# Kernel optimization log

Hardware: AMD Instinct MI355X
Metric: run time of the kernel (lower is better)

Reference implementation:

```python
import jax, jax.numpy as jnp
import numpy as np

B, S, D, H = 32, 512, 512, 8
DF = D // H  # dim_feature = 64
NEG_INF = -1e32


def setup_inputs() -> dict:
    key = jax.random.key(0)
    ks = jax.random.split(key, 8)
    std = 1.0 / np.sqrt(D)  # xavier-ish scale for square linears
    return {
        "q": jax.random.normal(ks[0], (B, S, D), jnp.float32),
        "k": jax.random.normal(ks[1], (B, S, D), jnp.float32),
        "v": jax.random.normal(ks[2], (B, S, D), jnp.float32),
        "mask": jnp.tril(jnp.ones((S, S), jnp.int32))[None, None],  # causal AKT mask
        "zero_pad": 1,
        "question_difficulty_emb": jax.random.normal(ks[3], (B, S, S), jnp.float32) * 0.1,
        "Wk": jax.random.normal(ks[4], (D, D), jnp.float32) * std,
        "bk": jnp.zeros((D,), jnp.float32),
        "Wv": jax.random.normal(ks[5], (D, D), jnp.float32) * std,
        "bv": jnp.zeros((D,), jnp.float32),
        "Wo": jax.random.normal(ks[6], (D, D), jnp.float32) * std,
        "bo": jnp.zeros((D,), jnp.float32),
        "gammas": jax.random.normal(ks[7], (H, 1, 1), jnp.float32) * 0.1,
    }


def reference(q, k, v, mask, zero_pad, question_difficulty_emb, Wk, bk, Wv, bv, Wo, bo, gammas):
    bs = q.shape[0]

    def proj(x, W, b):
        # Linear then split heads: [B,S,D] -> [B,H,S,DF]
        return (x @ W.T + b).reshape(bs, -1, H, DF).transpose(0, 2, 1, 3)

    qh = proj(q, Wk, bk)  # key_query_same=True: q uses key_linear
    kh = proj(k, Wk, bk)
    vh = proj(v, Wv, bv)

    scores = jnp.einsum("bhqd,bhkd->bhqk", qh, kh) / jnp.sqrt(jnp.float32(DF))
    seqlen = scores.shape[-1]
    maskb = mask == 0  # [1,1,S,S]

    # --- distance-decay term (computed under no_grad in torch, detached) ---
    scores_ = jax.nn.softmax(jnp.where(maskb, NEG_INF, scores), axis=-1)
    scores_ = scores_ * mask.astype(scores.dtype)
    distcum = jnp.cumsum(scores_, axis=-1)                      # [B,H,S,S]
    disttot = jnp.sum(scores_, axis=-1, keepdims=True)          # [B,H,S,1]
    pos = jnp.abs(jnp.arange(seqlen)[None, :] - jnp.arange(seqlen)[:, None]).astype(scores.dtype)
    dist_scores = jnp.sqrt(jnp.clip((disttot - distcum) * pos[None, None], 0.0))
    dist_scores = jax.lax.stop_gradient(dist_scores)

    gamma = -jax.nn.softplus(gammas)[None]                      # [1,H,1,1]
    diff = jnp.exp(jax.nn.sigmoid(question_difficulty_emb))[:, None]  # [B,1,S,S]
    total_effect = jnp.clip(jnp.exp(dist_scores * gamma * diff), 1e-5, 1e5)

    scores = scores * total_effect
    scores = jax.nn.softmax(jnp.where(maskb, NEG_INF, scores), axis=-1)
    if zero_pad:
        scores = scores.at[:, :, 0, :].set(0.0)  # zero first query row
    scores = jnp.where(maskb, 0.0, scores)
    # dropout p=0 (eval) -> identity

    out = jnp.einsum("bhqk,bhkd->bhqd", scores, vh)
    concat = out.transpose(0, 2, 1, 3).reshape(bs, -1, D)
    return concat @ Wo.T + bo
```

## Files before the change

kernel.cpp:

```cpp
#include <hip/hip_runtime.h>

typedef unsigned short u16;
typedef __attribute__((ext_vector_type(8))) short short8;
typedef __attribute__((ext_vector_type(4))) float f32x4;

__device__ __forceinline__ float b2f(u16 u) {
    return __uint_as_float(((unsigned int)u) << 16);
}
__device__ __forceinline__ u16 f2b(float f) {
    unsigned int x = __float_as_uint(f);
    return (u16)((x + 0x7FFFu + ((x >> 16) & 1u)) >> 16);
}
__device__ __forceinline__ float ldf(const void* p, size_t i, bool f32) {
    return f32 ? ((const float*)p)[i] : b2f(((const u16*)p)[i]);
}
__device__ __forceinline__ void stf(void* p, size_t i, bool f32, float v) {
    if (f32) ((float*)p)[i] = v; else ((u16*)p)[i] = f2b(v);
}

__global__ void detect_f32(const u16* __restrict__ q, int* __restrict__ flag) {
    __shared__ int cw, cz;
    if (threadIdx.x == 0) { cw = 0; cz = 0; }
    __syncthreads();
    int w = 0, z = 0;
    for (int i = threadIdx.x; i < 4096; i += 256) {
        u16 u = q[i];
        int e = (u >> 7) & 0xFF;
        if (e >= 0xC8) w++;
        if (((i & 1) == 0) && u == 0) z++;
    }
    atomicAdd(&cw, w); atomicAdd(&cz, z);
    __syncthreads();
    if (threadIdx.x == 0) *flag = (cw > 8 || cz > 1024) ? 1 : 0;
}

__global__ __launch_bounds__(256) void cvt_w3(
    const void* __restrict__ w0, const void* __restrict__ w1,
    const void* __restrict__ w2, u16* __restrict__ d0, u16* __restrict__ d1,
    u16* __restrict__ d2, int n, const int* __restrict__ flag)
{
    const bool f32 = (*flag) != 0;
    const int z = blockIdx.y;
    const void* src = (z == 0) ? w0 : (z == 1) ? w1 : w2;
    u16* dst = (z == 0) ? d0 : (z == 1) ? d1 : d2;
    const int i = (blockIdx.x * 256 + threadIdx.x) * 8;
    if (i >= n) return;
    short8 o;
    if (f32) {
        const float4* s = (const float4*)((const float*)src + i);
        float4 v0 = s[0], v1 = s[1];
        o[0] = (short)f2b(v0.x); o[1] = (short)f2b(v0.y);
        o[2] = (short)f2b(v0.z); o[3] = (short)f2b(v0.w);
        o[4] = (short)f2b(v1.x); o[5] = (short)f2b(v1.y);
        o[6] = (short)f2b(v1.z); o[7] = (short)f2b(v1.w);
    } else {
        o = *(const short8*)((const u16*)src + i);
    }
    *(short8*)(dst + i) = o;
}

#define BM 128
#define BN 128
#define BK 32
#define LSTR 40

template<int ASRC>
__device__ __forceinline__ void gemm_body(
    const void* __restrict__ A, const u16* __restrict__ W,
    const void* __restrict__ bias, void* __restrict__ dst,
    bool f32, int mode, int bm, int bn, int M, int N, int K)
{
    __shared__ u16 As[BM * LSTR];
    __shared__ u16 Bs[BN * LSTR];
    const int t = threadIdx.x;
    const int w = t >> 6, l = t & 63, lq = l & 15, quad = l >> 4;
    const int wr = (w >> 1) * 64, wc = (w & 1) * 64;
    const int srow = t >> 1;
    const int scol = (t & 1) * 16;

    f32x4 acc[4][4] = {};

    for (int k0 = 0; k0 < K; k0 += BK) {
        const size_t ai = (size_t)(bm + srow) * K + k0 + scol;
        short8 a0, a1;
        if (ASRC == 1 && f32) {
            const float4* ap = (const float4*)((const float*)A + ai);
            float4 f0 = ap[0], f1 = ap[1], f2 = ap[2], f3 = ap[3];
            a0[0] = (short)f2b(f0.x); a0[1] = (short)f2b(f0.y);
            a0[2] = (short)f2b(f0.z); a0[3] = (short)f2b(f0.w);
            a0[4] = (short)f2b(f1.x); a0[5] = (short)f2b(f1.y);
            a0[6] = (short)f2b(f1.z); a0[7] = (short)f2b(f1.w);
            a1[0] = (short)f2b(f2.x); a1[1] = (short)f2b(f2.y);
            a1[2] = (short)f2b(f2.z); a1[3] = (short)f2b(f2.w);
            a1[4] = (short)f2b(f3.x); a1[5] = (short)f2b(f3.y);
            a1[6] = (short)f2b(f3.z); a1[7] = (short)f2b(f3.w);
        } else {
            a0 = *(const short8*)((const u16*)A + ai);
            a1 = *(const short8*)((const u16*)A + ai + 8);
        }
        short8 b0 = *(const short8*)&W[(size_t)(bn + srow) * K + k0 + scol];
        short8 b1 = *(const short8*)&W[(size_t)(bn + srow) * K + k0 + scol + 8];
        __syncthreads();
        *(short8*)&As[srow * LSTR + scol]     = a0;
        *(short8*)&As[srow * LSTR + scol + 8] = a1;
        *(short8*)&Bs[srow * LSTR + scol]     = b0;
        *(short8*)&Bs[srow * LSTR + scol + 8] = b1;
        __syncthreads();
        short8 af[4], bf[4];
        #pragma unroll
        for (int i = 0; i < 4; ++i)
            af[i] = *(const short8*)&As[(wr + i * 16 + lq) * LSTR + quad * 8];
        #pragma unroll
        for (int j = 0; j < 4; ++j)
            bf[j] = *(const short8*)&Bs[(wc + j * 16 + lq) * LSTR + quad * 8];
        #pragma unroll
        for (int i = 0; i < 4; ++i)
            #pragma unroll
            for (int j = 0; j < 4; ++j)
                acc[i][j] = __builtin_amdgcn_mfma_f32_16x16x32_bf16(
                    af[i], bf[j], acc[i][j], 0, 0, 0);
    }

    #pragma unroll
    for (int j = 0; j < 4; ++j) {
        const int n = bn + wc + j * 16 + lq;
        const float bb = ldf(bias, n, f32);
        #pragma unroll
        for (int i = 0; i < 4; ++i) {
            #pragma unroll
            for (int r = 0; r < 4; ++r) {
                const int m = bm + wr + i * 16 + quad * 4 + r;
                const float vout = acc[i][j][r] + bb;
                if (mode == 0) {
                    const int b = m >> 9, s = m & 511, hh = n >> 6, df = n & 63;
                    ((u16*)dst)[((((size_t)b * 8 + hh) * 512 + s) << 6) + df] = f2b(vout);
                } else if (mode == 2) {
                    const int b = m >> 9, s = m & 511, hh = n >> 6, df = n & 63;
                    ((u16*)dst)[((((size_t)b * 8 + hh) * 64 + df) << 9) + s] = f2b(vout);
                } else {
                    stf(dst, (size_t)m * N + n, f32, vout);
                }
            }
        }
    }
}

__global__ __launch_bounds__(256) void proj3(
    const void* __restrict__ Aq, const void* __restrict__ Ak,
    const void* __restrict__ Av, const u16* __restrict__ cWk,
    const u16* __restrict__ cWv, const void* __restrict__ bk,
    const void* __restrict__ bv, u16* __restrict__ qh, u16* __restrict__ kh,
    u16* __restrict__ vt, const int* __restrict__ flag, int M, int N, int K)
{
    const bool f32 = (*flag) != 0;
    const int z = blockIdx.z;
    const void* A = (z == 0) ? Aq : (z == 1) ? Ak : Av;
    const u16* W = (z < 2) ? cWk : cWv;
    const void* bias = (z < 2) ? bk : bv;
    void* dst = (z == 0) ? (void*)qh : (z == 1) ? (void*)kh : (void*)vt;
    const int mode = (z < 2) ? 0 : 2;
    gemm_body<1>(A, W, bias, dst, f32, mode, blockIdx.y * BM, blockIdx.x * BN, M, N, K);
}

__global__ __launch_bounds__(256) void gemm_out(
    const u16* __restrict__ A, const u16* __restrict__ W,
    const void* __restrict__ bias, void* __restrict__ dst,
    const int* __restrict__ flag, int M, int N, int K)
{
    gemm_body<0>(A, W, bias, dst, (*flag) != 0, 1, blockIdx.y * BM, blockIdx.x * BN, M, N, K);
}

#define QT  16
#define SRS 577
#define PRS 584

__global__ __launch_bounds__(512) void akt_attn(
    const u16* __restrict__ qh, const u16* __restrict__ kh,
    const u16* __restrict__ vt, const void* __restrict__ qde,
    const void* __restrict__ gammas, const int* __restrict__ zero_pad,
    const int* __restrict__ flag, u16* __restrict__ attn)
{
    __shared__ _Float16 s_h[QT * SRS];
    __shared__ u16      p_lds[QT * PRS];

    const int blk = blockIdx.x;
    const int xcd = blk & 7;
    const int i0  = blk >> 3;
    const int qt  = i0 & 31;
    const int grp = i0 >> 5;
    const int h = xcd, b = grp;

    const int q0 = qt * QT;
    const int t = threadIdx.x, w = t >> 6, l = t & 63;
    const int lq = l & 15, quad = l >> 4;
    const bool f32 = (*flag) != 0;
    const size_t bh = ((size_t)b * 8 + h) * 512;
    const int qmax = q0 + QT - 1;

    {
        const u16* qb = qh + (bh + q0) * 64;
        short8 af0 = *(const short8*)(qb + lq * 64 +      quad * 8);
        short8 af1 = *(const short8*)(qb + lq * 64 + 32 + quad * 8);
        const u16* kb = kh + bh * 64;
        const int KT = (q0 + QT + 127) >> 7;
        int n0 = w * 16;
        bool act = (n0 <= qmax);
        short8 bf0, bf1;
        if (act) {
            bf0 = *(const short8*)(kb + (size_t)(n0 + lq) * 64 +      quad * 8);
            bf1 = *(const short8*)(kb + (size_t)(n0 + lq) * 64 + 32 + quad * 8);
        }
        for (int kt = 0; kt < KT; ++kt) {
            const int n0n = (kt + 1) * 128 + w * 16;
            const bool actn = (kt + 1 < KT) && (n0n <= qmax);
            short8 nb0, nb1;
            if (actn) {
                nb0 = *(const short8*)(kb + (size_t)(n0n + lq) * 64 +      quad * 8);
                nb1 = *(const short8*)(kb + (size_t)(n0n + lq) * 64 + 32 + quad * 8);
            }
            if (act) {
                f32x4 acc = {0.f, 0.f, 0.f, 0.f};
                acc = __builtin_amdgcn_mfma_f32_16x16x32_bf16(af0, bf0, acc, 0, 0, 0);
                acc = __builtin_amdgcn_mfma_f32_16x16x32_bf16(af1, bf1, acc, 0, 0, 0);
                const int col = n0 + lq;
                const int cm  = col + (col >> 3);
                #pragma unroll
                for (int r = 0; r < 4; ++r)
                    s_h[(quad * 4 + r) * SRS + cm] = (_Float16)(acc[r] * 0.125f);
            }
            bf0 = nb0; bf1 = nb1; act = actn; n0 = n0n;
        }
    }
    __syncthreads();

    {
        const float gma = -log1pf(expf(ldf(gammas, h, f32)));
        const int zp = zero_pad[0];
        const int c0 = l * 8;
        #pragma unroll
        for (int rr = 0; rr < 2; ++rr) {
            const int row = w * 2 + rr;
            const int q = q0 + row;
            const _Float16* srow = s_h + row * SRS + l * 9;
            float s[8];
            #pragma unroll
            for (int j = 0; j < 8; ++j)
                s[j] = (c0 + j <= q) ? (float)srow[j] : -1e30f;
            float cs[8]; float run = 0.f;
            #pragma unroll
            for (int j = 0; j < 8; ++j) { float p = __expf(s[j]); run += p; cs[j] = run; }
            float incl = run;
            #pragma unroll
            for (int o = 1; o < 64; o <<= 1) {
                float u = __shfl_up(incl, o, 64);
                if (l >= o) incl += u;
            }
            const float ls   = __shfl(incl, 63, 64);
            const float inv1 = __builtin_amdgcn_rcpf(ls);
            const float exclr = incl - run;
            float x[8];
            const size_t qoff = ((size_t)b * 512 + q) * 512 + c0;
            if (c0 <= q) {
                if (f32) {
                    const float* qp = (const float*)qde + qoff;
                    #pragma unroll
                    for (int j = 0; j < 8; ++j) x[j] = qp[j];
                } else {
                    short8 v8 = *(const short8*)((const u16*)qde + qoff);
                    #pragma unroll
                    for (int j = 0; j < 8; ++j) x[j] = b2f((u16)v8[j]);
                }
            } else {
                #pragma unroll
                for (int j = 0; j < 8; ++j) x[j] = 0.f;
            }
            float f8[8]; float lf = 0.f;
            #pragma unroll
            for (int j = 0; j < 8; ++j) {
                float dc   = (exclr + cs[j]) * inv1;
                float rem  = 1.f - dc;
                float pos  = (float)(q - (c0 + j));
                float dist = __builtin_amdgcn_sqrtf(fmaxf(rem * pos, 0.f));
                float sig  = __builtin_amdgcn_rcpf(1.f + __expf(-x[j]));
                float eff  = __expf(dist * gma * __expf(sig));
                eff = fminf(fmaxf(eff, 1e-5f), 1e5f);
                float s2 = (c0 + j <= q) ? s[j] * eff : -1e30f;
                float f = __expf(s2);
                f8[j] = f; lf += f;
            }
            #pragma unroll
            for (int o = 32; o > 0; o >>= 1) lf += __shfl_xor(lf, o, 64);
            float inv2 = __builtin_amdgcn_rcpf(lf);
            if (zp && q == 0) inv2 = 0.f;
            short8 pb;
            #pragma unroll
            for (int j = 0; j < 8; ++j) pb[j] = (short)f2b(f8[j] * inv2);
            *(short8*)(p_lds + row * PRS + c0 + 8 * (l >> 3)) = pb;
        }
    }
    __syncthreads();

    if (w < 4) {
        const int g = w;
        const int KS = (qmax >> 5) + 1;
        const u16* vb = vt + ((size_t)(b * 8 + h) * 64 + g * 16 + lq) * 512;
        const u16* prow = p_lds + lq * PRS;
        f32x4 oacc = {0.f, 0.f, 0.f, 0.f};
        int kb2 = quad * 8;
        short8 pa = *(const short8*)(prow + kb2 + 8 * (kb2 >> 6));
        short8 vv = *(const short8*)(vb + kb2);
        for (int ks = 0; ks < KS; ++ks) {
            short8 pan, vvn;
            const int kn = (ks + 1) * 32 + quad * 8;
            if (ks + 1 < KS) {
                pan = *(const short8*)(prow + kn + 8 * (kn >> 6));
                vvn = *(const short8*)(vb + kn);
            }
            oacc = __builtin_amdgcn_mfma_f32_16x16x32_bf16(pa, vv, oacc, 0, 0, 0);
            pa = pan; vv = vvn;
        }
        const size_t ob = ((size_t)b * 512 + q0 + quad * 4) * 512 + h * 64 + g * 16 + lq;
        #pragma unroll
        for (int r = 0; r < 4; ++r)
            attn[ob + (size_t)r * 512] = f2b(oacc[r]);
    }
}

extern "C" void kernel_launch(void* const* d_in, const int* in_sizes, int n_in,
                              void* d_out, int out_size, void* d_ws, size_t ws_size,
                              hipStream_t stream) {
    const void* q   = d_in[0];
    const void* k   = d_in[1];
    const void* v   = d_in[2];
    const int*  zp  = (const int*)d_in[4];
    const void* qde = d_in[5];
    const void* Wk  = d_in[6];
    const void* bk  = d_in[7];
    const void* Wv  = d_in[8];
    const void* bv  = d_in[9];
    const void* Wo  = d_in[10];
    const void* bo  = d_in[11];
    const void* gam = d_in[12];

    const int M = 32 * 512, N = 512, K = 512;
    const int NW = 512 * 512;

    char* ws = (char*)d_ws;
    int*  flag = (int*)ws;
    const size_t SZB = (size_t)M * K * 2;
    const size_t SZW = (size_t)NW * 2;
    u16* cWk  = (u16*)(ws + 1024);
    u16* cWv  = (u16*)(ws + 1024 + SZW);
    u16* cWo  = (u16*)(ws + 1024 + 2 * SZW);
    u16* qh   = (u16*)(ws + 1024 + 3 * SZW);
    u16* kh   = (u16*)(ws + 1024 + 3 * SZW + SZB);
    u16* vt   = (u16*)(ws + 1024 + 3 * SZW + 2 * SZB);
    u16* attn = (u16*)(ws + 1024 + 3 * SZW + 3 * SZB);

    detect_f32<<<1, 256, 0, stream>>>((const u16*)q, flag);
    cvt_w3<<<dim3(NW / 2048, 3), 256, 0, stream>>>(Wk, Wv, Wo, cWk, cWv, cWo, NW, flag);
    proj3<<<dim3(N / BN, M / BM, 3), 256, 0, stream>>>(
        q, k, v, cWk, cWv, bk, bv, qh, kh, vt, flag, M, N, K);
    akt_attn<<<8192, 512, 0, stream>>>(qh, kh, vt, qde, gam, zp, flag, attn);
    gemm_out<<<dim3(N / BN, M / BM), 256, 0, stream>>>(attn, cWo, bo, d_out, flag, M, N, K);
}
```

Measured before the change: 412.6 us.

## Pre-convert activations, use direct global-to-LDS loads, split PV across all waves

Adds a separate conversion pass that turns q/k/v into bf16 buffers. This lets the GEMM tiles load through global_load_lds straight into unpadded LDS, with no per-element conversion in registers. In the attention kernel, the difficulty-embedding load is hoisted and vectorized unconditionally, and the score LDS stride and padding scheme change. The PV matmul is split across all 8 waves, with the two partial sums reduced through shared memory. In exchange it costs an extra full read and write pass over the inputs, unpadded LDS tiles that may bank-conflict, and one more barrier.

```diff
diff --git a/kernel.cpp b/kernel.cpp
--- a/kernel.cpp
+++ b/kernel.cpp
@@ -2,6 +2,7 @@
 
 typedef unsigned short u16;
 typedef __attribute__((ext_vector_type(8))) short short8;
+typedef __attribute__((ext_vector_type(8))) _Float16 h8;
 typedef __attribute__((ext_vector_type(4))) float f32x4;
 
 __device__ __forceinline__ float b2f(u16 u) {
@@ -16,6 +17,12 @@
 }
 __device__ __forceinline__ void stf(void* p, size_t i, bool f32, float v) {
     if (f32) ((float*)p)[i] = v; else ((u16*)p)[i] = f2b(v);
+}
+
+__device__ __forceinline__ void ldsld16(const void* g, void* l) {
+    __builtin_amdgcn_global_load_lds(
+        (const __attribute__((address_space(1))) unsigned int*)g,
+        (__attribute__((address_space(3))) unsigned int*)l, 16, 0, 0);
 }
 
 __global__ void detect_f32(const u16* __restrict__ q, int* __restrict__ flag) {
@@ -34,14 +41,14 @@
     if (threadIdx.x == 0) *flag = (cw > 8 || cz > 1024) ? 1 : 0;
 }
 
-__global__ __launch_bounds__(256) void cvt_w3(
-    const void* __restrict__ w0, const void* __restrict__ w1,
-    const void* __restrict__ w2, u16* __restrict__ d0, u16* __restrict__ d1,
+__global__ __launch_bounds__(256) void cvt3(
+    const void* __restrict__ s0, const void* __restrict__ s1,
+    const void* __restrict__ s2, u16* __restrict__ d0, u16* __restrict__ d1,
     u16* __restrict__ d2, int n, const int* __restrict__ flag)
 {
     const bool f32 = (*flag) != 0;
-    const int z = blockIdx.y;
-    const void* src = (z == 0) ? w0 : (z == 1) ? w1 : w2;
+    const int z = blockIdx.z;
+    const void* src = (z == 0) ? s0 : (z == 1) ? s1 : s2;
     u16* dst = (z == 0) ? d0 : (z == 1) ? d1 : d2;
     const int i = (blockIdx.x * 256 + threadIdx.x) * 8;
     if (i >= n) return;
@@ -62,57 +69,42 @@
 #define BM 128
 #define BN 128
 #define BK 32
-#define LSTR 40
-
-template<int ASRC>
+
 __device__ __forceinline__ void gemm_body(
-    const void* __restrict__ A, const u16* __restrict__ W,
+    const u16* __restrict__ A, const u16* __restrict__ W,
     const void* __restrict__ bias, void* __restrict__ dst,
     bool f32, int mode, int bm, int bn, int M, int N, int K)
 {
-    __shared__ u16 As[BM * LSTR];
-    __shared__ u16 Bs[BN * LSTR];
+    __shared__ u16 As[BM * BK];
+    __shared__ u16 Bs[BN * BK];
     const int t = threadIdx.x;
     const int w = t >> 6, l = t & 63, lq = l & 15, quad = l >> 4;
     const int wr = (w >> 1) * 64, wc = (w & 1) * 64;
-    const int srow = t >> 1;
-    const int scol = (t & 1) * 16;
+
+    const int whalf = (w & 1) * 64;
+    const u16* gsrc = (w < 2) ? A : W;
+    const int  gbase = (w < 2) ? bm : bn;
+    u16* lbase = (w < 2) ? As : Bs;
 
     f32x4 acc[4][4] = {};
 
     for (int k0 = 0; k0 < K; k0 += BK) {
-        const size_t ai = (size_t)(bm + srow) * K + k0 + scol;
-        short8 a0, a1;
-        if (ASRC == 1 && f32) {
-            const float4* ap = (const float4*)((const float*)A + ai);
-            float4 f0 = ap[0], f1 = ap[1], f2 = ap[2], f3 = ap[3];
-            a0[0] = (short)f2b(f0.x); a0[1] = (short)f2b(f0.y);
-            a0[2] = (short)f2b(f0.z); a0[3] = (short)f2b(f0.w);
-            a0[4] = (short)f2b(f1.x); a0[5] = (short)f2b(f1.y);
-            a0[6] = (short)f2b(f1.z); a0[7] = (short)f2b(f1.w);
-            a1[0] = (short)f2b(f2.x); a1[1] = (short)f2b(f2.y);
-            a1[2] = (short)f2b(f2.z); a1[3] = (short)f2b(f2.w);
-            a1[4] = (short)f2b(f3.x); a1[5] = (short)f2b(f3.y);
-            a1[6] = (short)f2b(f3.z); a1[7] = (short)f2b(f3.w);
-        } else {
-            a0 = *(const short8*)((const u16*)A + ai);
-            a1 = *(const short8*)((const u16*)A + ai + 8);
-        }
-        short8 b0 = *(const short8*)&W[(size_t)(bn + srow) * K + k0 + scol];
-        short8 b1 = *(const short8*)&W[(size_t)(bn + srow) * K + k0 + scol + 8];
         __syncthreads();
-        *(short8*)&As[srow * LSTR + scol]     = a0;
-        *(short8*)&As[srow * LSTR + scol + 8] = a1;
-        *(short8*)&Bs[srow * LSTR + scol]     = b0;
-        *(short8*)&Bs[srow * LSTR + scol + 8] = b1;
+        #pragma unroll
+        for (int c = 0; c < 4; ++c) {
+            const int row = whalf + c * 16 + (l >> 2);
+            ldsld16(gsrc + (size_t)(gbase + row) * K + k0 + (l & 3) * 8,
+                    lbase + row * BK + (l & 3) * 8);
+        }
+        asm volatile("s_waitcnt vmcnt(0)" ::: "memory");
         __syncthreads();
         short8 af[4], bf[4];
         #pragma unroll
         for (int i = 0; i < 4; ++i)
-            af[i] = *(const short8*)&As[(wr + i * 16 + lq) * LSTR + quad * 8];
+            af[i] = *(const short8*)&As[(wr + i * 16 + lq) * BK + quad * 8];
         #pragma unroll
         for (int j = 0; j < 4; ++j)
-            bf[j] = *(const short8*)&Bs[(wc + j * 16 + lq) * LSTR + quad * 8];
+            bf[j] = *(const short8*)&Bs[(wc + j * 16 + lq) * BK + quad * 8];
         #pragma unroll
         for (int i = 0; i < 4; ++i)
             #pragma unroll
@@ -146,20 +138,19 @@
 }
 
 __global__ __launch_bounds__(256) void proj3(
-    const void* __restrict__ Aq, const void* __restrict__ Ak,
-    const void* __restrict__ Av, const u16* __restrict__ cWk,
+    const u16* __restrict__ cq, const u16* __restrict__ ck,
+    const u16* __restrict__ cv, const u16* __restrict__ cWk,
     const u16* __restrict__ cWv, const void* __restrict__ bk,
     const void* __restrict__ bv, u16* __restrict__ qh, u16* __restrict__ kh,
     u16* __restrict__ vt, const int* __restrict__ flag, int M, int N, int K)
 {
-    const bool f32 = (*flag) != 0;
     const int z = blockIdx.z;
-    const void* A = (z == 0) ? Aq : (z == 1) ? Ak : Av;
+    const u16* A = (z == 0) ? cq : (z == 1) ? ck : cv;
     const u16* W = (z < 2) ? cWk : cWv;
     const void* bias = (z < 2) ? bk : bv;
     void* dst = (z == 0) ? (void*)qh : (z == 1) ? (void*)kh : (void*)vt;
-    const int mode = (z < 2) ? 0 : 2;
-    gemm_body<1>(A, W, bias, dst, f32, mode, blockIdx.y * BM, blockIdx.x * BN, M, N, K);
+    gemm_body(A, W, bias, dst, (*flag) != 0, (z < 2) ? 0 : 2,
+              blockIdx.y * BM, blockIdx.x * BN, M, N, K);
 }
 
 __global__ __launch_bounds__(256) void gemm_out(
@@ -167,11 +158,12 @@
     const void* __restrict__ bias, void* __restrict__ dst,
     const int* __restrict__ flag, int M, int N, int K)
 {
-    gemm_body<0>(A, W, bias, dst, (*flag) != 0, 1, blockIdx.y * BM, blockIdx.x * BN, M, N, K);
+    gemm_body(A, W, bias, dst, (*flag) != 0, 1,
+              blockIdx.y * BM, blockIdx.x * BN, M, N, K);
 }
 
 #define QT  16
-#define SRS 577
+#define SRS 568
 #define PRS 584
 
 __global__ __launch_bounds__(512) void akt_attn(
@@ -184,11 +176,10 @@
     __shared__ u16      p_lds[QT * PRS];
 
     const int blk = blockIdx.x;
-    const int xcd = blk & 7;
-    const int i0  = blk >> 3;
-    const int qt  = i0 & 31;
-    const int grp = i0 >> 5;
-    const int h = xcd, b = grp;
+    const int h = blk & 7;
+    const int i0 = blk >> 3;
+    const int qt = i0 & 31;
+    const int b = i0 >> 5;
 
     const int q0 = qt * QT;
     const int t = threadIdx.x, w = t >> 6, l = t & 63;
@@ -222,8 +213,7 @@
                 f32x4 acc = {0.f, 0.f, 0.f, 0.f};
                 acc = __builtin_amdgcn_mfma_f32_16x16x32_bf16(af0, bf0, acc, 0, 0, 0);
                 acc = __builtin_amdgcn_mfma_f32_16x16x32_bf16(af1, bf1, acc, 0, 0, 0);
-                const int col = n0 + lq;
-                const int cm  = col + (col >> 3);
+                const int cm = n0 + lq + 8 * (n0 >> 6);
                 #pragma unroll
                 for (int r = 0; r < 4; ++r)
                     s_h[(quad * 4 + r) * SRS + cm] = (_Float16)(acc[r] * 0.125f);
@@ -241,11 +231,23 @@
         for (int rr = 0; rr < 2; ++rr) {
             const int row = w * 2 + rr;
             const int q = q0 + row;
-            const _Float16* srow = s_h + row * SRS + l * 9;
+            float x[8];
+            const size_t qoff = ((size_t)b * 512 + q) * 512 + c0;
+            if (f32) {
+                const float4* qp = (const float4*)((const float*)qde + qoff);
+                float4 x0 = qp[0], x1 = qp[1];
+                x[0] = x0.x; x[1] = x0.y; x[2] = x0.z; x[3] = x0.w;
+                x[4] = x1.x; x[5] = x1.y; x[6] = x1.z; x[7] = x1.w;
+            } else {
+                short8 v8 = *(const short8*)((const u16*)qde + qoff);
+                #pragma unroll
+                for (int j = 0; j < 8; ++j) x[j] = b2f((u16)v8[j]);
+            }
+            h8 sv = *(const h8*)(s_h + row * SRS + l * 8 + 8 * (l >> 3));
             float s[8];
             #pragma unroll
             for (int j = 0; j < 8; ++j)
-                s[j] = (c0 + j <= q) ? (float)srow[j] : -1e30f;
+                s[j] = (c0 + j <= q) ? (float)sv[j] : -1e30f;
             float cs[8]; float run = 0.f;
             #pragma unroll
             for (int j = 0; j < 8; ++j) { float p = __expf(s[j]); run += p; cs[j] = run; }
@@ -258,22 +260,6 @@
             const float ls   = __shfl(incl, 63, 64);
             const float inv1 = __builtin_amdgcn_rcpf(ls);
             const float exclr = incl - run;
-            float x[8];
-            const size_t qoff = ((size_t)b * 512 + q) * 512 + c0;
-            if (c0 <= q) {
-                if (f32) {
-                    const float* qp = (const float*)qde + qoff;
-                    #pragma unroll
-                    for (int j = 0; j < 8; ++j) x[j] = qp[j];
-                } else {
-                    short8 v8 = *(const short8*)((const u16*)qde + qoff);
-                    #pragma unroll
-                    for (int j = 0; j < 8; ++j) x[j] = b2f((u16)v8[j]);
-                }
-            } else {
-                #pragma unroll
-                for (int j = 0; j < 8; ++j) x[j] = 0.f;
-            }
             float f8[8]; float lf = 0.f;
             #pragma unroll
             for (int j = 0; j < 8; ++j) {
@@ -300,29 +286,33 @@
     }
     __syncthreads();
 
-    if (w < 4) {
-        const int g = w;
+    {
+        const int g = w & 3;
+        const int half = w >> 2;
         const int KS = (qmax >> 5) + 1;
         const u16* vb = vt + ((size_t)(b * 8 + h) * 64 + g * 16 + lq) * 512;
         const u16* prow = p_lds + lq * PRS;
         f32x4 oacc = {0.f, 0.f, 0.f, 0.f};
-        int kb2 = quad * 8;
-        short8 pa = *(const short8*)(prow + kb2 + 8 * (kb2 >> 6));
-        short8 vv = *(const short8*)(vb + kb2);
-        for (int ks = 0; ks < KS; ++ks) {
-            short8 pan, vvn;
-            const int kn = (ks + 1) * 32 + quad * 8;
-            if (ks + 1 < KS) {
-                pan = *(const short8*)(prow + kn + 8 * (kn >> 6));
-                vvn = *(const short8*)(vb + kn);
-            }
+        for (int ks = half; ks < KS; ks += 2) {
+            const int kb2 = ks * 32 + quad * 8;
+            short8 pa = *(const short8*)(prow + kb2 + 8 * (kb2 >> 6));
+            short8 vv = *(const short8*)(vb + kb2);
             oacc = __builtin_amdgcn_mfma_f32_16x16x32_bf16(pa, vv, oacc, 0, 0, 0);
-            pa = pan; vv = vvn;
-        }
-        const size_t ob = ((size_t)b * 512 + q0 + quad * 4) * 512 + h * 64 + g * 16 + lq;
-        #pragma unroll
-        for (int r = 0; r < 4; ++r)
-            attn[ob + (size_t)r * 512] = f2b(oacc[r]);
+        }
+        float* opart = (float*)s_h;
+        if (half == 1) {
+            #pragma unroll
+            for (int r = 0; r < 4; ++r)
+                opart[(g * 16 + quad * 4 + r) * 17 + lq] = oacc[r];
+        }
+        __syncthreads();
+        if (half == 0) {
+            const size_t ob = ((size_t)b * 512 + q0 + quad * 4) * 512 + h * 64 + g * 16 + lq;
+            #pragma unroll
+            for (int r = 0; r < 4; ++r)
+                attn[ob + (size_t)r * 512] =
+                    f2b(oacc[r] + opart[(g * 16 + quad * 4 + r) * 17 + lq]);
+        }
     }
 }
 
@@ -343,24 +333,29 @@
     const void* gam = d_in[12];
 
     const int M = 32 * 512, N = 512, K = 512;
+    const int NBIG = M * K;
     const int NW = 512 * 512;
 
     char* ws = (char*)d_ws;
-    int*  flag = (int*)ws;
-    const size_t SZB = (size_t)M * K * 2;
+    int* flag = (int*)ws;
+    const size_t SZB = (size_t)NBIG * 2;
     const size_t SZW = (size_t)NW * 2;
     u16* cWk  = (u16*)(ws + 1024);
     u16* cWv  = (u16*)(ws + 1024 + SZW);
     u16* cWo  = (u16*)(ws + 1024 + 2 * SZW);
-    u16* qh   = (u16*)(ws + 1024 + 3 * SZW);
-    u16* kh   = (u16*)(ws + 1024 + 3 * SZW + SZB);
-    u16* vt   = (u16*)(ws + 1024 + 3 * SZW + 2 * SZB);
-    u16* attn = (u16*)(ws + 1024 + 3 * SZW + 3 * SZB);
+    u16* cq   = (u16*)(ws + 1024 + 3 * SZW);
+    u16* ck   = (u16*)(ws + 1024 + 3 * SZW + SZB);
+    u16* cv   = (u16*)(ws + 1024 + 3 * SZW + 2 * SZB);
+    u16* qh   = (u16*)(ws + 1024 + 3 * SZW + 3 * SZB);
+    u16* kh   = (u16*)(ws + 1024 + 3 * SZW + 4 * SZB);
+    u16* vt   = (u16*)(ws + 1024 + 3 * SZW + 5 * SZB);
+    u16* attn = (u16*)(ws + 1024 + 3 * SZW + 6 * SZB);
 
     detect_f32<<<1, 256, 0, stream>>>((const u16*)q, flag);
-    cvt_w3<<<dim3(NW / 2048, 3), 256, 0, stream>>>(Wk, Wv, Wo, cWk, cWv, cWo, NW, flag);
+    cvt3<<<dim3(NW / 2048, 1, 3), 256, 0, stream>>>(Wk, Wv, Wo, cWk, cWv, cWo, NW, flag);
+    cvt3<<<dim3(NBIG / 2048, 1, 3), 256, 0, stream>>>(q, k, v, cq, ck, cv, NBIG, flag);
     proj3<<<dim3(N / BN, M / BM, 3), 256, 0, stream>>>(
-        q, k, v, cWk, cWv, bk, bv, qh, kh, vt, flag, M, N, K);
+        cq, ck, cv, cWk, cWv, bk, bv, qh, kh, vt, flag, M, N, K);
     akt_attn<<<8192, 512, 0, stream>>>(qh, kh, vt, qde, gam, zp, flag, attn);
     gemm_out<<<dim3(N / BN, M / BM), 256, 0, stream>>>(attn, cWo, bo, d_out, flag, M, N, K);
 }
```

Result: faster. 386.0 us (-6.4%).
